# Optimization experiments

Hardware: AMD Instinct MI355X
Metric: run time of the kernel (lower is better)

Reference implementation:

```python
import jax, jax.numpy as jnp
import numpy as np

N_SECTORS = 10          # = 1.0 / slice_range with normalized slice indices in [0, 1)
SLICE_RANGE = 0.1
PAIRWISE_EPS = 1e-6     # torch.nn.functional.pairwise_distance default eps (added to the diff)


def setup_inputs() -> dict:
    key = jax.random.key(0)
    k1, k2, k3, k4 = jax.random.split(key, 4)
    source_embeddings = jax.random.normal(k1, (200000, 256), dtype=jnp.float32)
    source_sectors = jax.random.randint(k2, (200000,), 0, N_SECTORS, dtype=jnp.int32)
    target_embeddings = jax.random.normal(k3, (100000, 256), dtype=jnp.float32)
    target_slice_idx = jax.random.uniform(k4, (100000,), dtype=jnp.float32)
    return {
        "source_embeddings": source_embeddings,
        "source_sectors": source_sectors,
        "target_embeddings": target_embeddings,
        "target_slice_idx": target_slice_idx,
    }


def reference(source_embeddings, source_sectors, target_embeddings, target_slice_idx):
    # cluster_centers[i] = mean of source_embeddings where source_sectors == i
    sums = jax.ops.segment_sum(source_embeddings, source_sectors, num_segments=N_SECTORS)  # [S, D]
    counts = jax.ops.segment_sum(
        jnp.ones((source_embeddings.shape[0],), dtype=source_embeddings.dtype),
        source_sectors, num_segments=N_SECTORS)                                            # [S]
    cluster_centers = sums / counts[:, None]                                               # [S, D]

    # get_sectors_from_index: bucket normalized slice index into sectors of width slice_range
    target_sectors = jnp.clip(
        jnp.floor(target_slice_idx / SLICE_RANGE).astype(jnp.int32), 0, N_SECTORS - 1)     # [N]

    cc = cluster_centers[target_sectors]                                                   # [N, D] gather

    # F.pairwise_distance with p=2, eps=1e-6: ||x1 - x2 + eps||_2
    diff = target_embeddings - cc + PAIRWISE_EPS
    distances = jnp.sqrt(jnp.sum(diff * diff, axis=-1))                                    # [N]
    return distances.mean()
```

## Files before the change

kernel.cpp:

```cpp
#include <hip/hip_runtime.h>
#include <math.h>

#define D      256
#define NSEC   10
#define EPS    1e-6f
#define SLICE  0.1f

#define WS_SUMS 0
#define WS_CNT  (NSEC * D)
#define WS_PART (NSEC * D + NSEC)
#define WS_ZERO_FLOATS (NSEC * D + NSEC)

__global__ void k_zero(float* __restrict__ ws) {
    int i = blockIdx.x * blockDim.x + threadIdx.x;
    if (i < WS_ZERO_FLOATS) ws[i] = 0.f;
}

__global__ __launch_bounds__(256) void k_sums(const float* __restrict__ emb,
                                              const int* __restrict__ sec,
                                              float* __restrict__ ws, int nrows) {
    const int lane = threadIdx.x & 63;
    const int wid  = threadIdx.x >> 6;
    const int gw   = blockIdx.x * 4 + wid;
    const int nw   = gridDim.x * 4;

    float4 acc[NSEC];
    float  cnt[NSEC];
#pragma unroll
    for (int s = 0; s < NSEC; ++s) { acc[s] = make_float4(0.f, 0.f, 0.f, 0.f); cnt[s] = 0.f; }

    const float* ep = emb + (size_t)lane * 4;

    auto accum = [&](int sv, float4 v) {
        const int s = __builtin_amdgcn_readfirstlane(sv);
#pragma unroll
        for (int ss = 0; ss < NSEC; ++ss) {
            if (s == ss) {
                acc[ss].x += v.x; acc[ss].y += v.y; acc[ss].z += v.z; acc[ss].w += v.w;
                cnt[ss] += 1.f;
            }
        }
    };

    int r = gw;
    for (; r + 3 * nw < nrows; r += 4 * nw) {
        const int s0 = sec[r];
        const int s1 = sec[r + nw];
        const int s2 = sec[r + 2 * nw];
        const int s3 = sec[r + 3 * nw];
        const float4 v0 = *reinterpret_cast<const float4*>(ep + (size_t)r * D);
        const float4 v1 = *reinterpret_cast<const float4*>(ep + (size_t)(r + nw) * D);
        const float4 v2 = *reinterpret_cast<const float4*>(ep + (size_t)(r + 2 * nw) * D);
        const float4 v3 = *reinterpret_cast<const float4*>(ep + (size_t)(r + 3 * nw) * D);
        accum(s0, v0); accum(s1, v1); accum(s2, v2); accum(s3, v3);
    }
    for (; r < nrows; r += nw)
        accum(sec[r], *reinterpret_cast<const float4*>(ep + (size_t)r * D));

    __shared__ float lsum[NSEC * D];
    __shared__ float lcnt[NSEC];
    for (int i = threadIdx.x; i < NSEC * D; i += 256) lsum[i] = 0.f;
    if (threadIdx.x < NSEC) lcnt[threadIdx.x] = 0.f;
    __syncthreads();

    for (int w = 0; w < 4; ++w) {
        if (wid == w) {
#pragma unroll
            for (int ss = 0; ss < NSEC; ++ss) {
                float* p = &lsum[ss * D + lane * 4];
                p[0] += acc[ss].x; p[1] += acc[ss].y; p[2] += acc[ss].z; p[3] += acc[ss].w;
                if (lane == 0) lcnt[ss] += cnt[ss];
            }
        }
        __syncthreads();
    }

#pragma unroll
    for (int ss = 0; ss < NSEC; ++ss)
        atomicAdd(&ws[WS_SUMS + ss * D + threadIdx.x], lsum[ss * D + threadIdx.x]);
    if (threadIdx.x < NSEC)
        atomicAdd(&ws[WS_CNT + threadIdx.x], lcnt[threadIdx.x]);
}

__global__ __launch_bounds__(256, 4) void k_dist4(const float* __restrict__ temb,
                                                  const float* __restrict__ tsl,
                                                  const float* __restrict__ ws,
                                                  float* __restrict__ part, int nrows) {
    __shared__ float lc[NSEC * D];
    for (int i = threadIdx.x; i < NSEC * D; i += 256) {
        const int s = i >> 8;
        lc[i] = ws[WS_SUMS + i] / ws[WS_CNT + s];
    }
    __syncthreads();

    const int lane = threadIdx.x & 63;
    const int wid  = threadIdx.x >> 6;
    const int gw   = blockIdx.x * 4 + wid;
    const int nw   = gridDim.x * 4;

    const float* tp = temb + (size_t)lane * 4;

    float wacc = 0.f;
    int r = gw;
    for (; r + 7 * nw < nrows; r += 8 * nw) {
        float  t[8];
        float4 v[8];
#pragma unroll
        for (int k = 0; k < 8; ++k) t[k] = tsl[r + k * nw];
#pragma unroll
        for (int k = 0; k < 8; ++k)
            v[k] = *reinterpret_cast<const float4*>(tp + (size_t)(r + k * nw) * D);

        asm volatile("" ::: "memory");

        float l[8];
#pragma unroll
        for (int k = 0; k < 8; ++k) {
            int s = (int)floorf(t[k] / SLICE);
            s = s < 0 ? 0 : (s > NSEC - 1 ? NSEC - 1 : s);
            const float4 c = *reinterpret_cast<const float4*>(&lc[s * D + lane * 4]);
            const float dx = v[k].x - c.x + EPS;
            const float dy = v[k].y - c.y + EPS;
            const float dz = v[k].z - c.z + EPS;
            const float dw = v[k].w - c.w + EPS;
            l[k] = dx * dx + dy * dy + dz * dz + dw * dw;
        }

#pragma unroll
        for (int off = 32; off >= 1; off >>= 1) {
#pragma unroll
            for (int k = 0; k < 8; ++k) l[k] += __shfl_xor(l[k], off, 64);
        }
#pragma unroll
        for (int k = 0; k < 8; ++k) wacc += sqrtf(l[k]);
    }
    for (; r < nrows; r += nw) {
        const float si = tsl[r];
        int s = (int)floorf(si / SLICE);
        s = s < 0 ? 0 : (s > NSEC - 1 ? NSEC - 1 : s);
        const float4 vv = *reinterpret_cast<const float4*>(tp + (size_t)r * D);
        const float4 c = *reinterpret_cast<const float4*>(&lc[s * D + lane * 4]);
        const float dx = vv.x - c.x + EPS;
        const float dy = vv.y - c.y + EPS;
        const float dz = vv.z - c.z + EPS;
        const float dw = vv.w - c.w + EPS;
        float loc = dx * dx + dy * dy + dz * dz + dw * dw;
#pragma unroll
        for (int off = 32; off >= 1; off >>= 1) loc += __shfl_xor(loc, off, 64);
        wacc += sqrtf(loc);
    }

    __shared__ float wsum[4];
    if (lane == 0) wsum[wid] = wacc;
    __syncthreads();
    if (threadIdx.x == 0)
        part[blockIdx.x] = wsum[0] + wsum[1] + wsum[2] + wsum[3];
}

__global__ __launch_bounds__(1024) void k_final(const float* __restrict__ part,
                                                float* __restrict__ out,
                                                int nparts, float invN) {
    float v = 0.f;
    for (int i = threadIdx.x; i < nparts; i += 1024) v += part[i];
#pragma unroll
    for (int off = 32; off >= 1; off >>= 1) v += __shfl_xor(v, off, 64);
    __shared__ float s16[16];
    if ((threadIdx.x & 63) == 0) s16[threadIdx.x >> 6] = v;
    __syncthreads();
    if (threadIdx.x == 0) {
        float tot = 0.f;
#pragma unroll
        for (int k = 0; k < 16; ++k) tot += s16[k];
        out[0] = tot * invN;
    }
}

extern "C" void kernel_launch(void* const* d_in, const int* in_sizes, int n_in,
                              void* d_out, int out_size, void* d_ws, size_t ws_size,
                              hipStream_t stream) {
    const float* semb = (const float*)d_in[0];
    const int*   ssec = (const int*)d_in[1];
    const float* temb = (const float*)d_in[2];
    const float* tsl  = (const float*)d_in[3];
    float* ws  = (float*)d_ws;
    float* out = (float*)d_out;
    const int nS = in_sizes[1];
    const int nT = in_sizes[3];

    hipLaunchKernelGGL(k_zero, dim3((WS_ZERO_FLOATS + 255) / 256), dim3(256), 0, stream, ws);
    hipLaunchKernelGGL(k_sums, dim3(1024), dim3(256), 0, stream, semb, ssec, ws, nS);
    hipLaunchKernelGGL(k_dist4, dim3(1024), dim3(256), 0, stream,
                       temb, tsl, ws, ws + WS_PART, nT);
    hipLaunchKernelGGL(k_final, dim3(1), dim3(1024), 0, stream,
                       ws + WS_PART, out, 1024, 1.0f / (float)nT);
}
```

Measured before the change: 103.0 us.

## Precompute negated centers, keep them in registers, transpose-reduce row sums via LDS

```diff
diff --git a/kernel.cpp b/kernel.cpp
--- a/kernel.cpp
+++ b/kernel.cpp
@@ -8,7 +8,8 @@
 
 #define WS_SUMS 0
 #define WS_CNT  (NSEC * D)
-#define WS_PART (NSEC * D + NSEC)
+#define WS_CC   (NSEC * D + NSEC)
+#define WS_PART (WS_CC + NSEC * D)
 #define WS_ZERO_FLOATS (NSEC * D + NSEC)
 
 __global__ void k_zero(float* __restrict__ ws) {
@@ -82,79 +83,94 @@
         atomicAdd(&ws[WS_CNT + threadIdx.x], lcnt[threadIdx.x]);
 }
 
-__global__ __launch_bounds__(256, 4) void k_dist4(const float* __restrict__ temb,
+__global__ __launch_bounds__(256) void k_cc(float* __restrict__ ws) {
+    const int t = threadIdx.x;
+    __shared__ float inv[NSEC];
+    if (t < NSEC) inv[t] = 1.f / ws[WS_CNT + t];
+    __syncthreads();
+#pragma unroll
+    for (int s = 0; s < NSEC; ++s)
+        ws[WS_CC + s * D + t] = EPS - ws[WS_SUMS + s * D + t] * inv[s];
+}
+
+__global__ __launch_bounds__(256, 4) void k_dist5(const float* __restrict__ temb,
                                                   const float* __restrict__ tsl,
                                                   const float* __restrict__ ws,
                                                   float* __restrict__ part, int nrows) {
-    __shared__ float lc[NSEC * D];
-    for (int i = threadIdx.x; i < NSEC * D; i += 256) {
-        const int s = i >> 8;
-        lc[i] = ws[WS_SUMS + i] / ws[WS_CNT + s];
-    }
-    __syncthreads();
-
     const int lane = threadIdx.x & 63;
     const int wid  = threadIdx.x >> 6;
     const int gw   = blockIdx.x * 4 + wid;
     const int nw   = gridDim.x * 4;
 
+    float4 cr[NSEC];
+#pragma unroll
+    for (int ss = 0; ss < NSEC; ++ss)
+        cr[ss] = *reinterpret_cast<const float4*>(&ws[WS_CC + ss * D + lane * 4]);
+
+    __shared__ float pl[4][32 * 65];
+    __shared__ float bsum[4];
+    float* P = pl[wid];
+
     const float* tp = temb + (size_t)lane * 4;
 
+    auto rowp = [&](int i, int ok, float si) -> void {};
+
     float wacc = 0.f;
-    int r = gw;
-    for (; r + 7 * nw < nrows; r += 8 * nw) {
-        float  t[8];
-        float4 v[8];
-#pragma unroll
-        for (int k = 0; k < 8; ++k) t[k] = tsl[r + k * nw];
-#pragma unroll
-        for (int k = 0; k < 8; ++k)
-            v[k] = *reinterpret_cast<const float4*>(tp + (size_t)(r + k * nw) * D);
-
-        asm volatile("" ::: "memory");
-
-        float l[8];
-#pragma unroll
-        for (int k = 0; k < 8; ++k) {
-            int s = (int)floorf(t[k] / SLICE);
-            s = s < 0 ? 0 : (s > NSEC - 1 ? NSEC - 1 : s);
-            const float4 c = *reinterpret_cast<const float4*>(&lc[s * D + lane * 4]);
-            const float dx = v[k].x - c.x + EPS;
-            const float dy = v[k].y - c.y + EPS;
-            const float dz = v[k].z - c.z + EPS;
-            const float dw = v[k].w - c.w + EPS;
-            l[k] = dx * dx + dy * dy + dz * dz + dw * dw;
+    for (int i0 = 0; gw + (size_t)i0 * nw < (size_t)nrows; i0 += 32) {
+#pragma unroll 1
+        for (int j = 0; j < 32; j += 4) {
+            int   rr[4], ok[4];
+            float t4[4];
+            float4 v4[4];
+#pragma unroll
+            for (int k = 0; k < 4; ++k) {
+                const int i = i0 + j + k;
+                const int r = gw + i * nw;
+                ok[k] = r < nrows;
+                rr[k] = ok[k] ? r : nrows - 1;
+                t4[k] = tsl[rr[k]];
+            }
+#pragma unroll
+            for (int k = 0; k < 4; ++k)
+                v4[k] = *reinterpret_cast<const float4*>(tp + (size_t)rr[k] * D);
+
+#pragma unroll
+            for (int k = 0; k < 4; ++k) {
+                int sv = (int)floorf(t4[k] / SLICE);
+                sv = sv < 0 ? 0 : (sv > NSEC - 1 ? NSEC - 1 : sv);
+                const int s = __builtin_amdgcn_readfirstlane(sv);
+                float p = 0.f;
+#pragma unroll
+                for (int ss = 0; ss < NSEC; ++ss) {
+                    if (s == ss) {
+                        const float dx = v4[k].x + cr[ss].x;
+                        const float dy = v4[k].y + cr[ss].y;
+                        const float dz = v4[k].z + cr[ss].z;
+                        const float dw = v4[k].w + cr[ss].w;
+                        p = dx * dx + dy * dy + dz * dz + dw * dw;
+                    }
+                }
+                p = ok[k] ? p : 0.f;
+                P[(j + k) * 65 + lane] = p;
+            }
         }
 
-#pragma unroll
-        for (int off = 32; off >= 1; off >>= 1) {
-#pragma unroll
-            for (int k = 0; k < 8; ++k) l[k] += __shfl_xor(l[k], off, 64);
-        }
-#pragma unroll
-        for (int k = 0; k < 8; ++k) wacc += sqrtf(l[k]);
-    }
-    for (; r < nrows; r += nw) {
-        const float si = tsl[r];
-        int s = (int)floorf(si / SLICE);
-        s = s < 0 ? 0 : (s > NSEC - 1 ? NSEC - 1 : s);
-        const float4 vv = *reinterpret_cast<const float4*>(tp + (size_t)r * D);
-        const float4 c = *reinterpret_cast<const float4*>(&lc[s * D + lane * 4]);
-        const float dx = vv.x - c.x + EPS;
-        const float dy = vv.y - c.y + EPS;
-        const float dz = vv.z - c.z + EPS;
-        const float dw = vv.w - c.w + EPS;
-        float loc = dx * dx + dy * dy + dz * dz + dw * dw;
-#pragma unroll
-        for (int off = 32; off >= 1; off >>= 1) loc += __shfl_xor(loc, off, 64);
-        wacc += sqrtf(loc);
-    }
-
-    __shared__ float wsum[4];
-    if (lane == 0) wsum[wid] = wacc;
+        const int lrow = lane & 31, half = lane >> 5;
+        float a = 0.f;
+        const float* Pr = &P[lrow * 65 + half * 32];
+#pragma unroll
+        for (int i = 0; i < 32; ++i) a += Pr[i];
+        a += __shfl_xor(a, 32, 64);
+        float d = (half == 0) ? sqrtf(a) : 0.f;
+#pragma unroll
+        for (int off = 16; off >= 1; off >>= 1) d += __shfl_xor(d, off, 64);
+        wacc += d;
+    }
+
+    if (lane == 0) bsum[wid] = wacc;
     __syncthreads();
     if (threadIdx.x == 0)
-        part[blockIdx.x] = wsum[0] + wsum[1] + wsum[2] + wsum[3];
+        part[blockIdx.x] = bsum[0] + bsum[1] + bsum[2] + bsum[3];
 }
 
 __global__ __launch_bounds__(1024) void k_final(const float* __restrict__ part,
@@ -189,7 +205,8 @@
 
     hipLaunchKernelGGL(k_zero, dim3((WS_ZERO_FLOATS + 255) / 256), dim3(256), 0, stream, ws);
     hipLaunchKernelGGL(k_sums, dim3(1024), dim3(256), 0, stream, semb, ssec, ws, nS);
-    hipLaunchKernelGGL(k_dist4, dim3(1024), dim3(256), 0, stream,
+    hipLaunchKernelGGL(k_cc, dim3(1), dim3(256), 0, stream, ws);
+    hipLaunchKernelGGL(k_dist5, dim3(1024), dim3(256), 0, stream,
                        temb, tsl, ws, ws + WS_PART, nT);
     hipLaunchKernelGGL(k_final, dim3(1), dim3(1024), 0, stream,
                        ws + WS_PART, out, 1024, 1.0f / (float)nT);
```

Measured after the change: 103.9 us. About the same (+0.9%).
